# Kernel optimization log

Measured on AMD Instinct MI355X. Metric: run time of the kernel, lower is better.

Reference implementation:

```python
import jax, jax.numpy as jnp
import numpy as np

T, B, E, H = 2048, 2, 1024, 16
HD = E // H

def setup_inputs() -> dict:
    key = jax.random.key(0)
    k1, k2, k3 = jax.random.split(key, 3)
    x = jax.random.normal(k1, (T, B, E), dtype=jnp.float32)
    # xavier-uniform-like scale for weights
    in_proj_w = jax.random.normal(k2, (3 * E, E), dtype=jnp.float32) * (2.0 / (4 * E)) ** 0.5
    in_proj_b = jnp.zeros((3 * E,), dtype=jnp.float32)
    out_w = jax.random.normal(k3, (E, E), dtype=jnp.float32) * (1.0 / E) ** 0.5
    out_b = jnp.zeros((E,), dtype=jnp.float32)
    return {"x": x, "in_proj_w": in_proj_w, "in_proj_b": in_proj_b, "out_w": out_w, "out_b": out_b}

def reference(x, in_proj_w, in_proj_b, out_w, out_b):
    t, b, e = x.shape
    scale = HD ** (-0.5)
    # fused QKV projection: F.linear(x, W, b) = x @ W.T + b
    qkv = x @ in_proj_w.T + in_proj_b            # [T, B, 3E]
    q, k, v = jnp.split(qkv, 3, axis=-1)         # each [T, B, E]
    q = q * scale
    # reshape to heads: [T, B, E] -> [B, H, T, HD]
    def to_heads(a):
        return a.reshape(t, b, H, HD).transpose(1, 2, 0, 3)
    qh, kh, vh = to_heads(q), to_heads(k), to_heads(v)
    # scores [B, H, T, T] -- full NxN materialization, same as torch.bmm
    scores = jnp.einsum('bhtd,bhsd->bhts', qh, kh)
    w = jax.nn.softmax(scores.astype(jnp.float32), axis=-1).astype(scores.dtype)
    attn = jnp.einsum('bhts,bhsd->bhtd', w, vh)  # [B, H, T, HD]
    attn = attn.transpose(2, 0, 1, 3).reshape(t, b, e)  # [T, B, E]
    attn = attn @ out_w.T + out_b
    attn_weights = w.sum(axis=1) / H             # [B, T, T] head-averaged
    return attn, attn_weights
```

## Files before the change

kernel.cpp:

```cpp
#include <hip/hip_runtime.h>
#include <hip/hip_bf16.h>
#include <cstdint>

#define T_DIM 2048
#define B_DIM 2
#define E_DIM 1024
#define H_DIM 16
#define HD_DIM 64
#define M_DIM 4096
#define N1_DIM 3072
#define QK_SCALE 0.125f

typedef __attribute__((ext_vector_type(8))) short bfrag;
typedef __attribute__((ext_vector_type(4))) float f32x4;

__device__ __forceinline__ short f2bf(float f) {
  union { float f; uint32_t u; } v; v.f = f;
  uint32_t r = v.u + 0x7fffu + ((v.u >> 16) & 1u);
  return (short)(r >> 16);
}
__device__ __forceinline__ float bf2f(short b) {
  union { uint32_t u; float f; } v; v.u = ((uint32_t)(uint16_t)b) << 16;
  return v.f;
}
__device__ __forceinline__ f32x4 mfma16(bfrag a, bfrag b, f32x4 c) {
  return __builtin_amdgcn_mfma_f32_16x16x32_bf16(a, b, c, 0, 0, 0);
}

__global__ void split_kernel(const float* __restrict__ in,
                             short* __restrict__ hi, short* __restrict__ lo, int n) {
  int i = blockIdx.x * blockDim.x + threadIdx.x;
  int stride = gridDim.x * blockDim.x;
  for (; i < n; i += stride) {
    float v = in[i];
    short h = f2bf(v);
    hi[i] = h;
    lo[i] = f2bf(v - bf2f(h));
  }
}

template<int N_T, int K_T, bool OUT_BF16, bool DO_SCALE>
__global__ __launch_bounds__(256) void gemm_split(
    const short* __restrict__ Ahi, const short* __restrict__ Alo,
    const short* __restrict__ Bhi, const short* __restrict__ Blo,
    const float* __restrict__ bias, void* __restrict__ Cout)
{
  constexpr int BK = 32;
  constexpr int LDT = BK + 8;
  __shared__ short As[2][128][LDT];
  __shared__ short Bs[2][128][LDT];

  const int m0 = blockIdx.y * 128;
  const int n0 = blockIdx.x * 128;
  const int tid = threadIdx.x;
  const int lane = tid & 63;
  const int wave = tid >> 6;
  const int wr = (wave >> 1) * 64;
  const int wc = (wave & 1) * 64;

  f32x4 acc[4][4];
#pragma unroll
  for (int i = 0; i < 4; ++i)
#pragma unroll
    for (int j = 0; j < 4; ++j) acc[i][j] = f32x4{0.f, 0.f, 0.f, 0.f};

  const int ldr = tid >> 1;
  const int ldc0 = (tid & 1) << 4;

  for (int k0 = 0; k0 < K_T; k0 += BK) {
    const size_t aoff = (size_t)(m0 + ldr) * K_T + k0 + ldc0;
    const size_t boff = (size_t)(n0 + ldr) * K_T + k0 + ldc0;
    bfrag ah0 = *(const bfrag*)(Ahi + aoff);
    bfrag ah1 = *(const bfrag*)(Ahi + aoff + 8);
    bfrag al0 = *(const bfrag*)(Alo + aoff);
    bfrag al1 = *(const bfrag*)(Alo + aoff + 8);
    bfrag bh0 = *(const bfrag*)(Bhi + boff);
    bfrag bh1 = *(const bfrag*)(Bhi + boff + 8);
    bfrag bl0 = *(const bfrag*)(Blo + boff);
    bfrag bl1 = *(const bfrag*)(Blo + boff + 8);
    __syncthreads();
    *(bfrag*)&As[0][ldr][ldc0]     = ah0;
    *(bfrag*)&As[0][ldr][ldc0 + 8] = ah1;
    *(bfrag*)&As[1][ldr][ldc0]     = al0;
    *(bfrag*)&As[1][ldr][ldc0 + 8] = al1;
    *(bfrag*)&Bs[0][ldr][ldc0]     = bh0;
    *(bfrag*)&Bs[0][ldr][ldc0 + 8] = bh1;
    *(bfrag*)&Bs[1][ldr][ldc0]     = bl0;
    *(bfrag*)&Bs[1][ldr][ldc0 + 8] = bl1;
    __syncthreads();

    const int fr = lane & 15;
    const int fk = (lane >> 4) << 3;
    bfrag afh[4], afl[4];
#pragma unroll
    for (int fi = 0; fi < 4; ++fi) {
      afh[fi] = *(const bfrag*)&As[0][wr + fi * 16 + fr][fk];
      afl[fi] = *(const bfrag*)&As[1][wr + fi * 16 + fr][fk];
    }
#pragma unroll
    for (int fj = 0; fj < 4; ++fj) {
      bfrag bfh = *(const bfrag*)&Bs[0][wc + fj * 16 + fr][fk];
      bfrag bfl = *(const bfrag*)&Bs[1][wc + fj * 16 + fr][fk];
#pragma unroll
      for (int fi = 0; fi < 4; ++fi) {
        acc[fi][fj] = mfma16(afh[fi], bfh, acc[fi][fj]);
        acc[fi][fj] = mfma16(afh[fi], bfl, acc[fi][fj]);
        acc[fi][fj] = mfma16(afl[fi], bfh, acc[fi][fj]);
      }
    }
  }

  const int cr = (lane >> 4) << 2;
  const int cc = lane & 15;
#pragma unroll
  for (int fi = 0; fi < 4; ++fi)
#pragma unroll
    for (int fj = 0; fj < 4; ++fj)
#pragma unroll
      for (int r = 0; r < 4; ++r) {
        int m = m0 + wr + fi * 16 + cr + r;
        int n = n0 + wc + fj * 16 + cc;
        float v = acc[fi][fj][r] + bias[n];
        if (DO_SCALE) { if (n < E_DIM) v *= QK_SCALE; }
        if (OUT_BF16) ((short*)Cout)[(size_t)m * N_T + n] = f2bf(v);
        else          ((float*)Cout)[(size_t)m * N_T + n] = v;
      }
}

__global__ __launch_bounds__(256) void attn_kernel(
    const short* __restrict__ qkv,
    float* __restrict__ linv_ws,
    short* __restrict__ ctx_hi, short* __restrict__ ctx_lo)
{
  __shared__ short Qs[64][72];
  __shared__ short Ks[64][72];
  __shared__ short Vt[64][72];
  __shared__ short Ps[64][72];
  __shared__ float l_lds[64];

  const int bh = blockIdx.x;
  const int b  = bh >> 4;
  const int h  = bh & 15;
  const int t0 = blockIdx.y * 64;
  const int tid  = threadIdx.x;
  const int lane = tid & 63;
  const int wave = tid >> 6;

  {
    int r = tid >> 2, ds = (tid & 3) << 4;
    const size_t base = ((size_t)(t0 + r) * B_DIM + b) * N1_DIM + h * HD_DIM + ds;
    *(bfrag*)&Qs[r][ds]     = *(const bfrag*)(qkv + base);
    *(bfrag*)&Qs[r][ds + 8] = *(const bfrag*)(qkv + base + 8);
  }
  if (tid < 64) l_lds[tid] = 0.0f;

  f32x4 pv[4];
#pragma unroll
  for (int i = 0; i < 4; ++i) pv[i] = f32x4{0.f, 0.f, 0.f, 0.f};

  const int fr = lane & 15;
  const int fk = (lane >> 4) << 3;

  for (int st = 0; st < T_DIM / 64; ++st) {
    const int s0 = st * 64;
    const int r = tid >> 2, ds = (tid & 3) << 4;
    const size_t kbase = ((size_t)(s0 + r) * B_DIM + b) * N1_DIM + E_DIM + h * HD_DIM + ds;
    const size_t vbase = kbase + E_DIM;
    bfrag kv0 = *(const bfrag*)(qkv + kbase);
    bfrag kv1 = *(const bfrag*)(qkv + kbase + 8);
    bfrag vv0 = *(const bfrag*)(qkv + vbase);
    bfrag vv1 = *(const bfrag*)(qkv + vbase + 8);
    __syncthreads();
    *(bfrag*)&Ks[r][ds]     = kv0;
    *(bfrag*)&Ks[r][ds + 8] = kv1;
#pragma unroll
    for (int j = 0; j < 8; ++j) Vt[ds + j][r]     = vv0[j];
#pragma unroll
    for (int j = 0; j < 8; ++j) Vt[ds + 8 + j][r] = vv1[j];
    __syncthreads();

    bfrag aq0 = *(const bfrag*)&Qs[wave * 16 + fr][fk];
    bfrag aq1 = *(const bfrag*)&Qs[wave * 16 + fr][fk + 32];
    f32x4 sacc[4];
#pragma unroll
    for (int fs = 0; fs < 4; ++fs) {
      bfrag bk0 = *(const bfrag*)&Ks[fs * 16 + fr][fk];
      bfrag bk1 = *(const bfrag*)&Ks[fs * 16 + fr][fk + 32];
      f32x4 a = f32x4{0.f, 0.f, 0.f, 0.f};
      a = mfma16(aq0, bk0, a);
      a = mfma16(aq1, bk1, a);
      sacc[fs] = a;
    }
    float rsum[4] = {0.f, 0.f, 0.f, 0.f};
#pragma unroll
    for (int fs = 0; fs < 4; ++fs) {
#pragma unroll
      for (int rr = 0; rr < 4; ++rr) {
        float p = __expf(sacc[fs][rr]);
        Ps[wave * 16 + ((lane >> 4) << 2) + rr][fs * 16 + fr] = f2bf(p);
        rsum[rr] += p;
      }
    }
#pragma unroll
    for (int rr = 0; rr < 4; ++rr) {
      float v = rsum[rr];
      v += __shfl_xor(v, 1);
      v += __shfl_xor(v, 2);
      v += __shfl_xor(v, 4);
      v += __shfl_xor(v, 8);
      if (fr == 0) l_lds[wave * 16 + ((lane >> 4) << 2) + rr] += v;
    }
    __syncthreads();

    bfrag pa0 = *(const bfrag*)&Ps[wave * 16 + fr][fk];
    bfrag pa1 = *(const bfrag*)&Ps[wave * 16 + fr][fk + 32];
#pragma unroll
    for (int fd = 0; fd < 4; ++fd) {
      bfrag bv0 = *(const bfrag*)&Vt[fd * 16 + fr][fk];
      bfrag bv1 = *(const bfrag*)&Vt[fd * 16 + fr][fk + 32];
      pv[fd] = mfma16(pa0, bv0, pv[fd]);
      pv[fd] = mfma16(pa1, bv1, pv[fd]);
    }
  }
  __syncthreads();

  if (tid < 64) linv_ws[(size_t)bh * T_DIM + t0 + tid] = 1.0f / l_lds[tid];
#pragma unroll
  for (int rr = 0; rr < 4; ++rr) {
    const int row = wave * 16 + ((lane >> 4) << 2) + rr;
    const float inv = 1.0f / l_lds[row];
#pragma unroll
    for (int fd = 0; fd < 4; ++fd) {
      float v = pv[fd][rr] * inv;
      int d = fd * 16 + fr;
      size_t off = ((size_t)(t0 + row) * B_DIM + b) * E_DIM + h * HD_DIM + d;
      short hi = f2bf(v);
      ctx_hi[off] = hi;
      ctx_lo[off] = f2bf(v - bf2f(hi));
    }
  }
}

__global__ __launch_bounds__(256) void weights_kernel(
    const short* __restrict__ qkv, const float* __restrict__ linv,
    float* __restrict__ outw)
{
  __shared__ short Qs[64][72];
  __shared__ short Ks[64][72];
  __shared__ float Ls[16][64];

  const int s0 = blockIdx.x * 64;
  const int bt = blockIdx.y;
  const int b  = bt >> 5;
  const int t0 = (bt & 31) * 64;
  const int tid  = threadIdx.x;
  const int lane = tid & 63;
  const int wave = tid >> 6;
  const int fr = lane & 15;
  const int fk = (lane >> 4) << 3;
  const int cr = (lane >> 4) << 2;

  {
    const int h  = tid >> 4;
    const int r4 = (tid & 15) << 2;
    float4 v = *(const float4*)(linv + (size_t)(b * H_DIM + h) * T_DIM + t0 + r4);
    Ls[h][r4 + 0] = v.x * (1.0f / H_DIM);
    Ls[h][r4 + 1] = v.y * (1.0f / H_DIM);
    Ls[h][r4 + 2] = v.z * (1.0f / H_DIM);
    Ls[h][r4 + 3] = v.w * (1.0f / H_DIM);
  }

  f32x4 wacc[4];
#pragma unroll
  for (int i = 0; i < 4; ++i) wacc[i] = f32x4{0.f, 0.f, 0.f, 0.f};

  const int r  = tid >> 2;
  const int ds = (tid & 3) << 4;

  for (int h = 0; h < H_DIM; ++h) {
    const size_t qbase = ((size_t)(t0 + r) * B_DIM + b) * N1_DIM + h * HD_DIM + ds;
    const size_t kbase = ((size_t)(s0 + r) * B_DIM + b) * N1_DIM + E_DIM + h * HD_DIM + ds;
    bfrag q0 = *(const bfrag*)(qkv + qbase);
    bfrag q1 = *(const bfrag*)(qkv + qbase + 8);
    bfrag k0 = *(const bfrag*)(qkv + kbase);
    bfrag k1 = *(const bfrag*)(qkv + kbase + 8);
    __syncthreads();
    *(bfrag*)&Qs[r][ds]     = q0;
    *(bfrag*)&Qs[r][ds + 8] = q1;
    *(bfrag*)&Ks[r][ds]     = k0;
    *(bfrag*)&Ks[r][ds + 8] = k1;
    __syncthreads();

    bfrag aq0 = *(const bfrag*)&Qs[wave * 16 + fr][fk];
    bfrag aq1 = *(const bfrag*)&Qs[wave * 16 + fr][fk + 32];
#pragma unroll
    for (int fs = 0; fs < 4; ++fs) {
      bfrag bk0 = *(const bfrag*)&Ks[fs * 16 + fr][fk];
      bfrag bk1 = *(const bfrag*)&Ks[fs * 16 + fr][fk + 32];
      f32x4 a = f32x4{0.f, 0.f, 0.f, 0.f};
      a = mfma16(aq0, bk0, a);
      a = mfma16(aq1, bk1, a);
#pragma unroll
      for (int rr = 0; rr < 4; ++rr)
        wacc[fs][rr] += __expf(a[rr]) * Ls[h][wave * 16 + cr + rr];
    }
  }

#pragma unroll
  for (int fs = 0; fs < 4; ++fs)
#pragma unroll
    for (int rr = 0; rr < 4; ++rr) {
      const int t = t0 + wave * 16 + cr + rr;
      outw[((size_t)b * T_DIM + t) * T_DIM + s0 + fs * 16 + fr] = wacc[fs][rr];
    }
}

extern "C" void kernel_launch(void* const* d_in, const int* in_sizes, int n_in,
                              void* d_out, int out_size, void* d_ws, size_t ws_size,
                              hipStream_t stream) {
  const float* x  = (const float*)d_in[0];
  const float* w1 = (const float*)d_in[1];
  const float* b1 = (const float*)d_in[2];
  const float* w2 = (const float*)d_in[3];
  const float* b2 = (const float*)d_in[4];
  float* out = (float*)d_out;

  char* ws = (char*)d_ws;
  size_t off = 0;
  auto carve = [&](size_t bytes) -> void* {
    void* p = ws + off;
    off = (off + bytes + 255) & ~(size_t)255;
    return p;
  };
  short* x_hi  = (short*)carve((size_t)M_DIM * E_DIM * 2);
  short* x_lo  = (short*)carve((size_t)M_DIM * E_DIM * 2);
  short* w1_hi = (short*)carve((size_t)N1_DIM * E_DIM * 2);
  short* w1_lo = (short*)carve((size_t)N1_DIM * E_DIM * 2);
  short* w2_hi = (short*)carve((size_t)E_DIM * E_DIM * 2);
  short* w2_lo = (short*)carve((size_t)E_DIM * E_DIM * 2);
  short* qkv   = (short*)carve((size_t)M_DIM * N1_DIM * 2);
  float* linv  = (float*)carve((size_t)B_DIM * H_DIM * T_DIM * 4);
  short* c_hi  = (short*)carve((size_t)M_DIM * E_DIM * 2);
  short* c_lo  = (short*)carve((size_t)M_DIM * E_DIM * 2);

  split_kernel<<<2048, 256, 0, stream>>>(x,  x_hi,  x_lo,  M_DIM * E_DIM);
  split_kernel<<<2048, 256, 0, stream>>>(w1, w1_hi, w1_lo, N1_DIM * E_DIM);
  split_kernel<<<1024, 256, 0, stream>>>(w2, w2_hi, w2_lo, E_DIM * E_DIM);

  gemm_split<N1_DIM, E_DIM, true, true><<<dim3(N1_DIM / 128, M_DIM / 128), 256, 0, stream>>>(
      x_hi, x_lo, w1_hi, w1_lo, b1, (void*)qkv);

  attn_kernel<<<dim3(B_DIM * H_DIM, T_DIM / 64), 256, 0, stream>>>(
      qkv, linv, c_hi, c_lo);

  weights_kernel<<<dim3(T_DIM / 64, B_DIM * (T_DIM / 64)), 256, 0, stream>>>(
      qkv, linv, out + (size_t)M_DIM * E_DIM);

  gemm_split<E_DIM, E_DIM, false, false><<<dim3(E_DIM / 128, M_DIM / 128), 256, 0, stream>>>(
      c_hi, c_lo, w2_hi, w2_lo, b2, (void*)out);
}
```

Before: 390.4 us.

## Prefetch K/V into registers, swizzle V-transpose LDS, drop Q LDS staging

The attention kernel now loads Q fragments straight from global memory into registers, so the Qs shared buffer and its per-iteration reads are gone. The next K/V tile is fetched into registers during the current tile's work, overlapping global latency with compute. The transposed V store into LDS uses an XOR swizzle to reduce bank conflicts. One __syncthreads between P writes and PV is removed, since each wave only reads its own Ps rows, and s_setprio is raised around the MFMA sections. Register pressure goes up, and dropping the barrier relies on that per-wave row ownership.

New measurement: 372.4 us. -4.6%, faster.

```diff
diff --git a/kernel.cpp b/kernel.cpp
--- a/kernel.cpp
+++ b/kernel.cpp
@@ -132,7 +132,6 @@
     float* __restrict__ linv_ws,
     short* __restrict__ ctx_hi, short* __restrict__ ctx_lo)
 {
-  __shared__ short Qs[64][72];
   __shared__ short Ks[64][72];
   __shared__ short Vt[64][72];
   __shared__ short Ps[64][72];
@@ -145,43 +144,44 @@
   const int tid  = threadIdx.x;
   const int lane = tid & 63;
   const int wave = tid >> 6;
-
-  {
-    int r = tid >> 2, ds = (tid & 3) << 4;
-    const size_t base = ((size_t)(t0 + r) * B_DIM + b) * N1_DIM + h * HD_DIM + ds;
-    *(bfrag*)&Qs[r][ds]     = *(const bfrag*)(qkv + base);
-    *(bfrag*)&Qs[r][ds + 8] = *(const bfrag*)(qkv + base + 8);
-  }
-  if (tid < 64) l_lds[tid] = 0.0f;
-
-  f32x4 pv[4];
-#pragma unroll
-  for (int i = 0; i < 4; ++i) pv[i] = f32x4{0.f, 0.f, 0.f, 0.f};
-
   const int fr = lane & 15;
   const int fk = (lane >> 4) << 3;
+  const int cr = (lane >> 4) << 2;
+
+  const size_t qb = ((size_t)(t0 + wave * 16 + fr) * B_DIM + b) * N1_DIM + h * HD_DIM;
+  const bfrag aq0 = *(const bfrag*)(qkv + qb + fk);
+  const bfrag aq1 = *(const bfrag*)(qkv + qb + fk + 32);
+
+  if (tid < 64) l_lds[tid] = 0.0f;
+
+  f32x4 pv[4];
+#pragma unroll
+  for (int i = 0; i < 4; ++i) pv[i] = f32x4{0.f, 0.f, 0.f, 0.f};
+
+  const int r  = tid >> 2;
+  const int ds = (tid & 3) << 4;
+  const int vc0 = (((r >> 3) ^ (ds >> 3)) << 3) | (r & 7);
+  const int vc1 = (((r >> 3) ^ ((ds >> 3) + 1)) << 3) | (r & 7);
+
+  const size_t kstep = ((size_t)64 * B_DIM) * N1_DIM;
+  size_t kb = ((size_t)r * B_DIM + b) * N1_DIM + E_DIM + h * HD_DIM + ds;
+  bfrag kv0 = *(const bfrag*)(qkv + kb);
+  bfrag kv1 = *(const bfrag*)(qkv + kb + 8);
+  bfrag vv0 = *(const bfrag*)(qkv + kb + E_DIM);
+  bfrag vv1 = *(const bfrag*)(qkv + kb + E_DIM + 8);
 
   for (int st = 0; st < T_DIM / 64; ++st) {
-    const int s0 = st * 64;
-    const int r = tid >> 2, ds = (tid & 3) << 4;
-    const size_t kbase = ((size_t)(s0 + r) * B_DIM + b) * N1_DIM + E_DIM + h * HD_DIM + ds;
-    const size_t vbase = kbase + E_DIM;
-    bfrag kv0 = *(const bfrag*)(qkv + kbase);
-    bfrag kv1 = *(const bfrag*)(qkv + kbase + 8);
-    bfrag vv0 = *(const bfrag*)(qkv + vbase);
-    bfrag vv1 = *(const bfrag*)(qkv + vbase + 8);
     __syncthreads();
     *(bfrag*)&Ks[r][ds]     = kv0;
     *(bfrag*)&Ks[r][ds + 8] = kv1;
 #pragma unroll
-    for (int j = 0; j < 8; ++j) Vt[ds + j][r]     = vv0[j];
-#pragma unroll
-    for (int j = 0; j < 8; ++j) Vt[ds + 8 + j][r] = vv1[j];
-    __syncthreads();
-
-    bfrag aq0 = *(const bfrag*)&Qs[wave * 16 + fr][fk];
-    bfrag aq1 = *(const bfrag*)&Qs[wave * 16 + fr][fk + 32];
+    for (int j = 0; j < 8; ++j) Vt[ds + j][vc0]     = vv0[j];
+#pragma unroll
+    for (int j = 0; j < 8; ++j) Vt[ds + 8 + j][vc1] = vv1[j];
+    __syncthreads();
+
     f32x4 sacc[4];
+    __builtin_amdgcn_s_setprio(1);
 #pragma unroll
     for (int fs = 0; fs < 4; ++fs) {
       bfrag bk0 = *(const bfrag*)&Ks[fs * 16 + fr][fk];
@@ -191,13 +191,23 @@
       a = mfma16(aq1, bk1, a);
       sacc[fs] = a;
     }
+    __builtin_amdgcn_s_setprio(0);
+
+    if (st + 1 < T_DIM / 64) {
+      kb += kstep;
+      kv0 = *(const bfrag*)(qkv + kb);
+      kv1 = *(const bfrag*)(qkv + kb + 8);
+      vv0 = *(const bfrag*)(qkv + kb + E_DIM);
+      vv1 = *(const bfrag*)(qkv + kb + E_DIM + 8);
+    }
+
     float rsum[4] = {0.f, 0.f, 0.f, 0.f};
 #pragma unroll
     for (int fs = 0; fs < 4; ++fs) {
 #pragma unroll
       for (int rr = 0; rr < 4; ++rr) {
         float p = __expf(sacc[fs][rr]);
-        Ps[wave * 16 + ((lane >> 4) << 2) + rr][fs * 16 + fr] = f2bf(p);
+        Ps[wave * 16 + cr + rr][fs * 16 + fr] = f2bf(p);
         rsum[rr] += p;
       }
     }
@@ -208,26 +218,29 @@
       v += __shfl_xor(v, 2);
       v += __shfl_xor(v, 4);
       v += __shfl_xor(v, 8);
-      if (fr == 0) l_lds[wave * 16 + ((lane >> 4) << 2) + rr] += v;
-    }
-    __syncthreads();
+      if (fr == 0) l_lds[wave * 16 + cr + rr] += v;
+    }
 
     bfrag pa0 = *(const bfrag*)&Ps[wave * 16 + fr][fk];
     bfrag pa1 = *(const bfrag*)&Ps[wave * 16 + fr][fk + 32];
+    __builtin_amdgcn_s_setprio(1);
 #pragma unroll
     for (int fd = 0; fd < 4; ++fd) {
-      bfrag bv0 = *(const bfrag*)&Vt[fd * 16 + fr][fk];
-      bfrag bv1 = *(const bfrag*)&Vt[fd * 16 + fr][fk + 32];
+      const int R = fd * 16 + fr;
+      const int sg = (R >> 3) & 7;
+      bfrag bv0 = *(const bfrag*)&Vt[R][(((fk >> 3) ^ sg) << 3)];
+      bfrag bv1 = *(const bfrag*)&Vt[R][((((fk >> 3) + 4) ^ sg) << 3)];
       pv[fd] = mfma16(pa0, bv0, pv[fd]);
       pv[fd] = mfma16(pa1, bv1, pv[fd]);
     }
+    __builtin_amdgcn_s_setprio(0);
   }
   __syncthreads();
 
   if (tid < 64) linv_ws[(size_t)bh * T_DIM + t0 + tid] = 1.0f / l_lds[tid];
 #pragma unroll
   for (int rr = 0; rr < 4; ++rr) {
-    const int row = wave * 16 + ((lane >> 4) << 2) + rr;
+    const int row = wave * 16 + cr + rr;
     const float inv = 1.0f / l_lds[row];
 #pragma unroll
     for (int fd = 0; fd < 4; ++fd) {
```
